# Performance work log

Hardware: AMD Instinct MI355X
Metric: run time of the kernel (lower is better)

## Reference

```python
import jax, jax.numpy as jnp
import numpy as np

B, J, I = 16, 96, 96
E, H = 256, 512
VS, VT = 32000, 32000
MAX_JUMP = 96
SJ = 2 * MAX_JUMP + 1  # 193
ALPHA_P0 = 0.3


def _lstm(x, W, b, reverse=False):
    """TF LSTMCell (gate order i, j, f, o; forget_bias=1.0). x: [B,J,E] -> [B,J,H]."""
    h_dim = W.shape[1] // 4
    xs = jnp.swapaxes(x, 0, 1)  # [J,B,E]
    if reverse:
        xs = xs[::-1]

    def step(carry, xt):
        h, c = carry
        z = jnp.concatenate([xt, h], axis=-1) @ W + b  # [B,4H]
        i, g, f, o = jnp.split(z, 4, axis=-1)
        c = jax.nn.sigmoid(f + 1.0) * c + jax.nn.sigmoid(i) * jnp.tanh(g)
        h = jax.nn.sigmoid(o) * jnp.tanh(c)
        return (h, c), h

    init = (jnp.zeros((x.shape[0], h_dim), x.dtype), jnp.zeros((x.shape[0], h_dim), x.dtype))
    _, hs = jax.lax.scan(step, init, xs)
    if reverse:
        hs = hs[::-1]
    return jnp.swapaxes(hs, 0, 1)


def setup_inputs() -> dict:
    key = jax.random.key(0)
    ks = jax.random.split(key, 16)
    s = 0.05
    return {
        "sources": jax.random.randint(ks[0], (B, I), 0, VS, dtype=jnp.int32),
        "targets": jax.random.randint(ks[1], (B, J), 0, VT, dtype=jnp.int32),
        "targets_null": jnp.array([VT - 1], dtype=jnp.int32),
        "emb": jax.random.normal(ks[2], (VT, E), jnp.float32) * s,
        "W_fw": jax.random.normal(ks[3], (E + H, 4 * H), jnp.float32) * s,
        "b_fw": jnp.zeros((4 * H,), jnp.float32),
        "W_bw": jax.random.normal(ks[4], (E + H, 4 * H), jnp.float32) * s,
        "b_bw": jnp.zeros((4 * H,), jnp.float32),
        "W_lstm": jax.random.normal(ks[5], (2 * H, E), jnp.float32) * s,
        "W1": jax.random.normal(ks[6], (E, H), jnp.float32) * s,
        "b1": jnp.zeros((H,), jnp.float32),
        "Wv": jax.random.normal(ks[7], (H, VS), jnp.float32) * s,
        "bv": jnp.zeros((VS,), jnp.float32),
        "Wj": jax.random.normal(ks[8], (H, SJ), jnp.float32) * s,
        "bj": jnp.zeros((SJ,), jnp.float32),
        "Wp": jax.random.normal(ks[9], (H, 1), jnp.float32) * s,
        "bp": jnp.zeros((1,), jnp.float32),
    }


def reference(sources, targets, targets_null, emb, W_fw, b_fw, W_bw, b_bw,
              W_lstm, W1, b1, Wv, bv, Wj, bj, Wp, bp):
    # shared target encoder (emission & transition use the same variables)
    e_word = emb[targets]          # [B,J,E]
    e_null = emb[targets_null]     # [1,E]
    h_fw = _lstm(e_word, W_fw, b_fw, reverse=False)
    h_bw = _lstm(e_word, W_bw, b_bw, reverse=True)
    ts = jnp.concatenate([h_fw, h_bw], axis=-1) @ W_lstm   # [B,J,E]
    ts = jnp.tanh(ts @ W1 + b1)                            # [B,J,H]
    tn = jnp.tanh(e_null @ W1 + b1)                        # [1,H]
    # keep_prob = 1.0 -> dropout is identity

    # ---- emission ----
    p_word = jax.nn.softmax(ts @ Wv + bv, axis=-1)         # [B,J,VS]
    p_null = jax.nn.softmax(tn @ Wv + bv, axis=-1)         # [1,VS]
    em_word = jnp.take_along_axis(p_word, sources[:, None, :], axis=2)  # [B,J,I]
    em_null = jnp.broadcast_to(p_null[0][sources][:, None, :], em_word.shape)  # tile over J
    emission_prob = jnp.concatenate([em_word, em_null], axis=1)  # [B,2J,I]

    # ---- transition ----
    jw = jax.nn.softmax(ts @ Wj + bj, axis=-1)             # [B,J,SJ]
    p0_scalar = jax.nn.sigmoid(tn @ Wp + bp)[0, 0] * ALPHA_P0
    p0 = jnp.broadcast_to(p0_scalar, (targets.shape[0], targets.shape[1]))  # [B,J]

    j_idx = jnp.arange(J)
    # window indices: for target word j, gather jw[j, MAX_JUMP - j + i] for i in [0,J)
    idx = MAX_JUMP - j_idx[:, None] + j_idx[None, :]       # [J,J]
    jww = jnp.take_along_axis(jw, idx[None, :, :], axis=2)  # [B,J,J]
    jww_sum = jnp.sum(jww, axis=-1, keepdims=True)
    jww_n = jww * (1.0 - p0[:, :, None]) / jww_sum          # normalized non-null jumps

    eye = jnp.eye(J, dtype=jww.dtype)
    half = jnp.concatenate([jww_n, p0[:, :, None] * eye], axis=2)       # [B,J,2J]
    transition = jnp.concatenate([half, half], axis=1)                  # [B,2J,2J]
    lhalf = jnp.concatenate([jnp.log(jww_n), jnp.log(p0)[:, :, None] * eye], axis=2)
    transition_log = jnp.concatenate([lhalf, lhalf], axis=1)            # [B,2J,2J]

    return emission_prob, transition, transition_log
```

## Files before the change

### kernel.cpp

```cpp
#include <hip/hip_runtime.h>
#include <math.h>

#define B_ 16
#define J_ 96
#define I_ 96
#define E_ 256
#define H_ 512
#define VS_ 32000
#define SJ_ 193
#define NROW (B_*J_)

typedef __attribute__((ext_vector_type(8))) short short8;
typedef __attribute__((ext_vector_type(4))) float f32x4;
typedef __attribute__((ext_vector_type(4))) unsigned int u32x4;

__device__ __forceinline__ float sigf(float x){ return 1.f/(1.f+__expf(-x)); }

__device__ __forceinline__ unsigned short f2bf(float x){
  unsigned int u = __float_as_uint(x);
  unsigned int r = (u + 0x7FFFu + ((u>>16)&1u)) >> 16;
  return (unsigned short)r;
}

#define ASYNC16(gp, lp) __builtin_amdgcn_global_load_lds( \
    (const __attribute__((address_space(1))) unsigned int*)(gp), \
    (__attribute__((address_space(3))) unsigned int*)(lp), 16, 0, 0)

__global__ void k_init(unsigned int* __restrict__ hex, float* __restrict__ rowsum){
  int i = blockIdx.x*256 + threadIdx.x;
  if (i < 32768) hex[i] = 0u;
  if (i < NROW + 1) rowsum[i] = 0.f;
}

__global__ void k_embed(const int* __restrict__ targets, const float* __restrict__ emb,
                        unsigned short* __restrict__ e_word_h){
  int row = blockIdx.x;
  int t = targets[row];
  e_word_h[(long long)row*E_ + threadIdx.x] = f2bf(emb[(long long)t*E_ + threadIdx.x]);
}

__device__ __forceinline__ void wtr_tile(const float* __restrict__ src,
                                         unsigned short* __restrict__ dst,
                                         int ldN, int nmax, int K, int n0, int k0,
                                         float* __restrict__ tile )
{
  const int t = threadIdx.x;
  #pragma unroll
  for (int rep = 0; rep < 8; rep++){
    int idx = rep*512 + t;
    int kk = idx >> 6, nn = idx & 63;
    tile[kk*65 + nn] = (n0+nn < nmax) ? src[(long long)(k0+kk)*ldN + n0 + nn] : 0.f;
  }
  __syncthreads();
  #pragma unroll
  for (int rep = 0; rep < 8; rep++){
    int idx = rep*512 + t;
    int nn = idx >> 6, kk = idx & 63;
    dst[(long long)(n0+nn)*K + k0 + kk] = f2bf(tile[kk*65 + nn]);
  }
}

__global__ __launch_bounds__(512, 2) void k_wtr2(const float* __restrict__ Wfw,
                                                 const float* __restrict__ Wbw,
                                                 unsigned short* __restrict__ WT){
  __shared__ float tile[64*65];
  int y = blockIdx.y;
  const float* src = y ? Wbw : Wfw;
  unsigned short* dst = WT + (long long)y*2048*256;
  int sid = blockIdx.x;
  int n0 = (sid & 31)*64, k0 = (sid >> 5)*64;
  wtr_tile(src, dst, 2048, 2048, 256, n0, k0, tile);
}

template<int MODE>
__global__ __launch_bounds__(256, 2) void k_bgemm(
    const unsigned short* __restrict__ Ah,
    const unsigned short* __restrict__ Bh,
    int K, int ncols,
    const float* __restrict__ bias,
    float* __restrict__ Cf,
    unsigned short* __restrict__ Ch,
    int ldc,
    float* __restrict__ rowsum)
{
  __shared__ unsigned short As[128*32];
  __shared__ unsigned short Bs[128*32];
  int nwg = gridDim.x;
  int braw = blockIdx.x;
  int wg = (braw & 7)*(nwg >> 3) + (braw >> 3);
  int mt = wg % 12, nt = wg / 12;
  const int m0 = mt*128, n0 = nt*128;
  const int t = threadIdx.x;
  const int lane = t & 63, w = t >> 6;
  const int wm = (w >> 1)*64, wn = (w & 1)*64;
  f32x4 acc[4][4] = {};
  for (int k0 = 0; k0 < K; k0 += 32){
    #pragma unroll
    for (int p = 0; p < 2; p++){
      int rowA = p*64 + (t >> 2);
      int kc = (t & 3) ^ ((rowA >> 1) & 3);
      const unsigned short* ga = Ah + (long long)(m0 + rowA)*K + k0 + kc*8;
      const unsigned short* gb = Bh + (long long)(n0 + rowA)*K + k0 + kc*8;
      unsigned short* la = As + p*2048 + w*512;
      unsigned short* lb = Bs + p*2048 + w*512;
      ASYNC16(ga, la);
      ASYNC16(gb, lb);
    }
    __syncthreads();
    short8 af[4], bf[4];
    const int rr = lane & 15, kch = lane >> 4;
    #pragma unroll
    for (int mi = 0; mi < 4; mi++){
      int rowA = wm + mi*16 + rr;
      int slot = kch ^ ((rowA >> 1) & 3);
      af[mi] = *(const short8*)&As[rowA*32 + slot*8];
    }
    #pragma unroll
    for (int ni = 0; ni < 4; ni++){
      int rowB = wn + ni*16 + rr;
      int slot = kch ^ ((rowB >> 1) & 3);
      bf[ni] = *(const short8*)&Bs[rowB*32 + slot*8];
    }
    #pragma unroll
    for (int mi = 0; mi < 4; mi++)
      #pragma unroll
      for (int ni = 0; ni < 4; ni++)
        acc[mi][ni] = __builtin_amdgcn_mfma_f32_16x16x32_bf16(af[mi], bf[ni], acc[mi][ni], 0, 0, 0);
    __syncthreads();
  }
  #pragma unroll
  for (int mi = 0; mi < 4; mi++){
    #pragma unroll
    for (int r = 0; r < 4; r++){
      int row = m0 + wm + mi*16 + ((lane >> 4) << 2) + r;
      if (MODE == 3){
        float s = 0.f;
        #pragma unroll
        for (int ni = 0; ni < 4; ni++){
          int col = n0 + wn + ni*16 + (lane & 15);
          s += __expf(acc[mi][ni][r] + bias[col]);
        }
        s += __shfl_xor(s, 1);
        s += __shfl_xor(s, 2);
        s += __shfl_xor(s, 4);
        s += __shfl_xor(s, 8);
        if ((lane & 15) == 0) atomicAdd(&rowsum[row], s);
      } else {
        #pragma unroll
        for (int ni = 0; ni < 4; ni++){
          int col = n0 + wn + ni*16 + (lane & 15);
          if (col >= ncols) continue;
          float v = acc[mi][ni][r] + (bias ? bias[col] : 0.f);
          if (MODE == 0){ Cf[(long long)row*ldc + col] = v; }
          if (MODE == 2){
            v = tanhf(v);
            if (Cf) Cf[(long long)row*ldc + col] = v;
            Ch[(long long)row*ldc + col] = f2bf(v);
          }
        }
      }
    }
  }
}

__global__ __launch_bounds__(512, 1) void k_fused(
    const float* __restrict__ Xfw, const float* __restrict__ Xbw,
    const float* __restrict__ Wfw, const float* __restrict__ Wbw,
    unsigned int* __restrict__ hex32,
    unsigned short* __restrict__ Hcat_h,
    const int* __restrict__ tnull, const float* __restrict__ emb,
    const float* __restrict__ W1, const float* __restrict__ b1,
    const float* __restrict__ Wp, const float* __restrict__ bp,
    const float* __restrict__ Wv, const float* __restrict__ bv,
    unsigned short* __restrict__ WvT,
    float* __restrict__ lognull, float* __restrict__ nullsum,
    float* __restrict__ p0,
    const float* __restrict__ Wl, unsigned short* __restrict__ W_comboT,
    const float* __restrict__ Wj, unsigned short* __restrict__ WjT)
{
  __shared__ __align__(16) unsigned short W_s[64*512];
  __shared__ __align__(16) float z_s[2][8][16][68];
  const int bid = blockIdx.x;
  const int t = threadIdx.x;

  if (bid >= 64){
    float* zflat = &z_s[0][0][0][0];
    int sid = bid - 64;
    if (sid == 0){
      float* en  = zflat;
      float* red = zflat + 256;
      if (t < E_) en[t] = emb[(long long)tnull[0]*E_ + t];
      __syncthreads();
      float s = b1[t];
      for (int e = 0; e < E_; e++) s += en[e]*W1[(long long)e*H_ + t];
      red[t] = tanhf(s)*Wp[t];
      __syncthreads();
      for (int w = 256; w > 0; w >>= 1){
        if (t < w) red[t] += red[t+w];
        __syncthreads();
      }
      if (t == 0) p0[0] = sigf(red[0] + bp[0])*0.3f;
      return;
    }
    sid -= 1;
    if (sid < 128){
      const int K8 = sid*8;
      float* WlS = zflat;
      #pragma unroll
      for (int rep = 0; rep < 4; rep++){
        int id = rep*512 + t;
        int kl = id >> 8, e = id & 255;
        WlS[kl*256 + e] = Wl[(long long)(K8 + kl)*256 + e];
      }
      __syncthreads();
      float acc[8] = {};
      for (int e = 0; e < 256; e++){
        float w1v = W1[(long long)e*512 + t];
        #pragma unroll
        for (int j = 0; j < 8; j++) acc[j] += WlS[j*256 + e]*w1v;
      }
      #pragma unroll
      for (int j = 0; j < 8; j++)
        W_comboT[(long long)t*1024 + K8 + j] = f2bf(acc[j]);
      return;
    }
    sid -= 128;
    if (sid < 32){
      wtr_tile(Wj, WjT, SJ_, SJ_, 512, (sid & 3)*64, (sid >> 2)*64, zflat);
      return;
    }
    sid -= 32;
    if (sid < 63){
      float* en  = zflat;
      float* tns = zflat + 256;
      float* red = zflat + 768;
      if (t < E_) en[t] = emb[(long long)tnull[0]*E_ + t];
      __syncthreads();
      float s0 = b1[t];
      for (int e = 0; e < E_; e++) s0 += en[e]*W1[(long long)e*H_ + t];
      tns[t] = tanhf(s0);
      __syncthreads();
      int c = sid*512 + t;
      float p = 0.f;
      if (c < VS_){
        float s = bv[c];
        for (int k = 0; k < H_; k++) s += tns[k]*Wv[(long long)k*VS_ + c];
        lognull[c] = s;
        p = __expf(s);
      }
      red[t] = p;
      __syncthreads();
      for (int w = 256; w > 0; w >>= 1){
        if (t < w) red[t] += red[t+w];
        __syncthreads();
      }
      if (t == 0) atomicAdd(nullsum, red[0]);
      return;
    }
    sid -= 63;
    wtr_tile(Wv, WvT, VS_, VS_, H_, (sid % 500)*64, (sid / 500)*64, zflat);
    return;
  }

  const int dir = bid >> 5;
  const int slice = bid & 31;
  const int u0 = slice * 16;
  const int lane = t & 63;
  const int w = t >> 6;
  const int m = lane & 15, hi = lane >> 4;
  const float* X = dir ? Xbw : Xfw;
  const float* Wg = (dir ? Wbw : Wfw) + (long long)E_*2048;
  char* hexd = (char*)hex32 + dir*65536;

  for (int rep = 0; rep < 8; rep++){
    int id = rep*512 + t;
    int k = id >> 3, col8 = (id & 7)*8;
    int g = col8 >> 4, uu0 = col8 & 15;
    const float* src = Wg + (long long)k*2048 + g*512 + u0 + uu0;
    float4 w0 = *(const float4*)src;
    float4 w1 = *(const float4*)(src + 4);
    float wv8[8] = {w0.x,w0.y,w0.z,w0.w,w1.x,w1.y,w1.z,w1.w};
    #pragma unroll
    for (int j = 0; j < 8; j++){
      int c = col8 + j;
      int byte = (c << 10) + (k << 1);
      byte ^= ((c & 7) << 4);
      *(unsigned short*)((char*)W_s + byte) = f2bf(wv8[j]);
    }
  }
  __syncthreads();

  short8 bfr[4][2];
  #pragma unroll
  for (int nt = 0; nt < 4; nt++)
    #pragma unroll
    for (int ck = 0; ck < 2; ck++){
      int col = nt*16 + m;
      int kc = 2*w + ck;
      int byte = (col << 10) + kc*64 + hi*16;
      byte ^= ((col & 7) << 4);
      bfr[nt][ck] = *(const short8*)((const char*)W_s + byte);
    }

  const int eb = t >> 4, eu = t & 15;
  float creg = 0.f;

  for (int step = 0; step < J_; step++){
    const int par = step & 1;
    const int t_eff = dir ? (J_-1-step) : step;
    float xg0=0.f, xg1=0.f, xg2=0.f, xg3=0.f;
    if (t < 256){
      const float* xr = X + ((long long)eb*J_ + t_eff)*2048 + u0 + eu;
      xg0 = xr[0]; xg1 = xr[512]; xg2 = xr[1024]; xg3 = xr[1536];
      asm volatile("" : "+v"(xg0), "+v"(xg1), "+v"(xg2), "+v"(xg3));
    }
    const char* ap = hexd + par*32768 + m*2048 + w*256 + hi*32;
    u32x4 d0, d1, d2, d3;
    const unsigned expt = (unsigned)step;
    unsigned spin = 0;
    for (;;){
      asm volatile("global_load_dwordx4 %0, %1, off sc0 sc1" : "=v"(d0) : "v"(ap));
      asm volatile("global_load_dwordx4 %0, %1, off offset:16 sc0 sc1" : "=v"(d1) : "v"(ap));
      asm volatile("global_load_dwordx4 %0, %1, off offset:128 sc0 sc1" : "=v"(d2) : "v"(ap));
      asm volatile("global_load_dwordx4 %0, %1, off offset:144 sc0 sc1" : "=v"(d3) : "v"(ap));
      asm volatile("s_waitcnt vmcnt(0)" ::: "memory");
      unsigned bad = (d0[1]^expt)|(d0[3]^expt)|(d1[1]^expt)|(d1[3]^expt)
                   | (d2[1]^expt)|(d2[3]^expt)|(d3[1]^expt)|(d3[3]^expt);
      if (__all(bad == 0u)) break;
      if (++spin > 65536u) break;
      __builtin_amdgcn_s_sleep(1);
    }
    __builtin_amdgcn_sched_barrier(0);
    union { unsigned int u[4]; short8 s; } a0, a1;
    a0.u[0]=d0[0]; a0.u[1]=d0[2]; a0.u[2]=d1[0]; a0.u[3]=d1[2];
    a1.u[0]=d2[0]; a1.u[1]=d2[2]; a1.u[2]=d3[0]; a1.u[3]=d3[2];
    f32x4 acc[4] = {{0.f,0.f,0.f,0.f},{0.f,0.f,0.f,0.f},{0.f,0.f,0.f,0.f},{0.f,0.f,0.f,0.f}};
    #pragma unroll
    for (int nt = 0; nt < 4; nt++){
      acc[nt] = __builtin_amdgcn_mfma_f32_16x16x32_bf16(a0.s, bfr[nt][0], acc[nt], 0,0,0);
      acc[nt] = __builtin_amdgcn_mfma_f32_16x16x32_bf16(a1.s, bfr[nt][1], acc[nt], 0,0,0);
    }
    #pragma unroll
    for (int nt = 0; nt < 4; nt++)
      #pragma unroll
      for (int r = 0; r < 4; r++)
        z_s[par][w][hi*4 + r][nt*16 + m] = acc[nt][r];
    __syncthreads();
    if (t < 256){
      float z0 = xg0, z1 = xg1, z2 = xg2, z3 = xg3;
      #pragma unroll
      for (int ke = 0; ke < 8; ke++){
        z0 += z_s[par][ke][eb][eu];
        z1 += z_s[par][ke][eb][16 + eu];
        z2 += z_s[par][ke][eb][32 + eu];
        z3 += z_s[par][ke][eb][48 + eu];
      }
      creg = sigf(z2 + 1.f)*creg + sigf(z0)*tanhf(z1);
      float hh = sigf(z3)*tanhf(creg);
      unsigned int hb16 = (unsigned int)f2bf(hh);
      unsigned int nb = (unsigned int)__shfl_xor((int)hb16, 1);
      if (!(eu & 1)){
        unsigned long long pkt = (unsigned long long)((hb16 & 0xffffu) | (nb << 16))
                               | ((unsigned long long)(unsigned)(step+1) << 32);
        __hip_atomic_store((unsigned long long*)(hexd + (par^1)*32768 + eb*2048 + (u0 + eu)*4),
                           pkt, __ATOMIC_RELAXED, __HIP_MEMORY_SCOPE_AGENT);
      }
      Hcat_h[((long long)eb*J_ + t_eff)*1024 + dir*512 + u0 + eu] = (unsigned short)hb16;
    }
  }
}

__global__ __launch_bounds__(64, 8) void k_glgemm(
    const unsigned short* __restrict__ t1h,
    const unsigned short* __restrict__ WvT,
    const float* __restrict__ bv,
    const int* __restrict__ sources,
    const float* __restrict__ rowsum,
    float* __restrict__ out_em)
{
  const int bx = blockIdx.x;
  const int b = bx / 36, tile = bx % 36;
  const int mt = tile / 6, nt = tile % 6;
  const int lane = threadIdx.x;
  const int rr = lane & 15, kq = lane >> 4;
  int s = sources[b*96 + nt*16 + rr];
  float bg = bv[s];
  const unsigned short* arow = t1h + ((long long)(b*96 + mt*16 + rr))*512 + kq*8;
  const unsigned short* brow = WvT + (long long)s*512 + kq*8;
  f32x4 acc = {0.f,0.f,0.f,0.f};
  #pragma unroll
  for (int kc = 0; kc < 16; kc++){
    short8 af = *(const short8*)(arow + kc*32);
    short8 bf = *(const short8*)(brow + kc*32);
    acc = __builtin_amdgcn_mfma_f32_16x16x32_bf16(af, bf, acc, 0, 0, 0);
  }
  #pragma unroll
  for (int r = 0; r < 4; r++){
    int j = mt*16 + kq*4 + r;
    int i = nt*16 + rr;
    float v = __expf(acc[r] + bg) / rowsum[b*96 + j];
    out_em[((long long)b*192 + j)*96 + i] = v;
  }
}

__global__ void k_emission_null(const float* __restrict__ lognull,
                                const float* __restrict__ nullsum,
                                const int* __restrict__ sources,
                                float* __restrict__ out_em){
  int b = blockIdx.x;
  int i = threadIdx.x;
  if (i >= 96) return;
  int s = sources[b*96 + i];
  float v = __expf(lognull[s]) / nullsum[0];
  for (int jj = 0; jj < 96; jj++)
    out_em[((long long)b*192 + 96 + jj)*96 + i] = v;
}

__global__ void k_transition(const float* __restrict__ jlog, const float* __restrict__ p0p,
                             float* __restrict__ T, float* __restrict__ TL){
  int bx = blockIdx.x;
  int b = bx / J_, j = bx % J_;
  int tid = threadIdx.x;
  __shared__ float ex[128];
  __shared__ float red[128];
  float e = 0.f;
  if (tid < 96) e = __expf(jlog[(long long)bx*SJ_ + (96 - j + tid)]);
  ex[tid] = e; red[tid] = e;
  __syncthreads();
  for (int w = 64; w > 0; w >>= 1){
    if (tid < w) red[tid] += red[tid+w];
    __syncthreads();
  }
  float p0 = p0p[0];
  float scale = (1.f - p0) / red[0];
  float lp0 = logf(p0);
  long long r0 = ((long long)b*192 + j)*192;
  long long r1 = ((long long)b*192 + j + 96)*192;
  for (int col = tid; col < 192; col += 128){
    float tv, lv;
    if (col < 96){ tv = ex[col]*scale; lv = logf(tv); }
    else { bool d = (col - 96) == j; tv = d ? p0 : 0.f; lv = d ? lp0 : 0.f; }
    T[r0 + col] = tv; T[r1 + col] = tv;
    TL[r0 + col] = lv; TL[r1 + col] = lv;
  }
}

extern "C" void kernel_launch(void* const* d_in, const int* in_sizes, int n_in,
                              void* d_out, int out_size, void* d_ws, size_t ws_size,
                              hipStream_t stream)
{
  const int* sources = (const int*)d_in[0];
  const int* targets = (const int*)d_in[1];
  const int* tnull   = (const int*)d_in[2];
  const float* emb   = (const float*)d_in[3];
  const float* Wfw   = (const float*)d_in[4];
  const float* bfw   = (const float*)d_in[5];
  const float* Wbw   = (const float*)d_in[6];
  const float* bbw   = (const float*)d_in[7];
  const float* Wl    = (const float*)d_in[8];
  const float* W1    = (const float*)d_in[9];
  const float* b1    = (const float*)d_in[10];
  const float* Wv    = (const float*)d_in[11];
  const float* bv    = (const float*)d_in[12];
  const float* Wj    = (const float*)d_in[13];
  const float* bj    = (const float*)d_in[14];
  const float* Wp    = (const float*)d_in[15];
  const float* bp    = (const float*)d_in[16];
  float* out = (float*)d_out;
  float* ws  = (float*)d_ws;

  long long off = 0;
  float* Xfw    = ws + off; off += (long long)NROW*2048;
  float* Xbw    = ws + off; off += (long long)NROW*2048;
  unsigned short* e_word_h = (unsigned short*)(ws + off); off += (long long)NROW*E_/2;
  unsigned short* WT       = (unsigned short*)(ws + off); off += 2LL*2048*256/2;
  unsigned short* Hcat_h   = (unsigned short*)(ws + off); off += (long long)NROW*1024/2;
  unsigned int* hex32 = (unsigned int*)(ws + off); off += 32768;
  unsigned short* t1h = (unsigned short*)(ws + off); off += (long long)NROW*H_/2;
  unsigned short* W_comboT = (unsigned short*)(ws + off); off += 512LL*1024/2;
  unsigned short* WjT      = (unsigned short*)(ws + off); off += 256LL*512/2;
  float* rowsum = ws + off; off += NROW;
  float* nullsum= ws + off; off += 1;
  float* p0     = ws + off; off += 1;
  float* lognull= ws + off; off += VS_;
  float* jlog   = ws + off; off += (long long)NROW*SJ_;
  unsigned short* WvT = (unsigned short*)(ws + off); off += (long long)VS_*H_/2;

  float* out_em = out;
  float* out_T  = out + (long long)B_*192*96;
  float* out_TL = out_T + (long long)B_*192*192;

  k_init<<<128, 256, 0, stream>>>(hex32, rowsum);

  k_embed<<<NROW, 256, 0, stream>>>(targets, emb, e_word_h);
  k_wtr2<<<dim3(128, 2), 512, 0, stream>>>(Wfw, Wbw, WT);

  k_bgemm<0><<<192, 256, 0, stream>>>(e_word_h, WT,            E_, 2048, bfw, Xfw, nullptr, 2048, nullptr);
  k_bgemm<0><<<192, 256, 0, stream>>>(e_word_h, WT + 2048*256, E_, 2048, bbw, Xbw, nullptr, 2048, nullptr);

  k_fused<<<4288, 512, 0, stream>>>(Xfw, Xbw, Wfw, Wbw, hex32, Hcat_h,
                                    tnull, emb, W1, b1, Wp, bp, Wv, bv,
                                    WvT, lognull, nullsum, p0,
                                    Wl, W_comboT, Wj, WjT);

  k_bgemm<2><<<48, 256, 0, stream>>>(Hcat_h, W_comboT, 2*H_, H_, b1, nullptr, t1h, H_, nullptr);

  k_bgemm<0><<<24, 256, 0, stream>>>(t1h, WjT, H_, SJ_, bj, jlog, nullptr, SJ_, nullptr);

  k_bgemm<3><<<3000, 256, 0, stream>>>(t1h, WvT, H_, VS_, bv, nullptr, nullptr, VS_, rowsum);

  k_glgemm<<<576, 64, 0, stream>>>(t1h, WvT, bv, sources, rowsum, out_em);

  k_emission_null<<<B_, 128, 0, stream>>>(lognull, nullsum, sources, out_em);
  k_transition<<<NROW, 128, 0, stream>>>(jlog, p0, out_T, out_TL);
}
```

Before: 483.5 us.

## Merge small launches into fused head, mega GEMM, and final kernels; double-buffer spin poll

Collapses init, embed, and weight-transpose into one head kernel, and batches the two input-projection GEMMs into a single 2D launch. The jump GEMM, vocab row-sum GEMM, and gathered emission GEMM now share one mega launch, and the null-emission and transition kernels merge into one final kernel that also applies the softmax normalization. The LSTM spin-wait loop now keeps two sets of loads in flight so polling overlaps with the flag check. The aim is to cut launch count and tail idle time. The cost is that division by rowsum moves to a separate read-modify-write pass over the emission output.

Result: slower. 565.3 us (+16.9%).

```diff
diff --git a/kernel.cpp b/kernel.cpp
--- a/kernel.cpp
+++ b/kernel.cpp
@@ -26,23 +26,31 @@
     (const __attribute__((address_space(1))) unsigned int*)(gp), \
     (__attribute__((address_space(3))) unsigned int*)(lp), 16, 0, 0)
 
-__global__ void k_init(unsigned int* __restrict__ hex, float* __restrict__ rowsum){
-  int i = blockIdx.x*256 + threadIdx.x;
-  if (i < 32768) hex[i] = 0u;
-  if (i < NROW + 1) rowsum[i] = 0.f;
-}
-
-__global__ void k_embed(const int* __restrict__ targets, const float* __restrict__ emb,
-                        unsigned short* __restrict__ e_word_h){
-  int row = blockIdx.x;
-  int t = targets[row];
-  e_word_h[(long long)row*E_ + threadIdx.x] = f2bf(emb[(long long)t*E_ + threadIdx.x]);
+__device__ __forceinline__ void wtr_tile256(const float* __restrict__ src,
+                                            unsigned short* __restrict__ dst,
+                                            int ldN, int nmax, int K, int n0, int k0,
+                                            float* __restrict__ tile )
+{
+  const int t = threadIdx.x;
+  #pragma unroll
+  for (int rep = 0; rep < 16; rep++){
+    int idx = rep*256 + t;
+    int kk = idx >> 6, nn = idx & 63;
+    tile[kk*65 + nn] = (n0+nn < nmax) ? src[(long long)(k0+kk)*ldN + n0 + nn] : 0.f;
+  }
+  __syncthreads();
+  #pragma unroll
+  for (int rep = 0; rep < 16; rep++){
+    int idx = rep*256 + t;
+    int nn = idx >> 6, kk = idx & 63;
+    dst[(long long)(n0+nn)*K + k0 + kk] = f2bf(tile[kk*65 + nn]);
+  }
 }
 
 __device__ __forceinline__ void wtr_tile(const float* __restrict__ src,
                                          unsigned short* __restrict__ dst,
                                          int ldN, int nmax, int K, int n0, int k0,
-                                         float* __restrict__ tile )
+                                         float* __restrict__ tile)
 {
   const int t = threadIdx.x;
   #pragma unroll
@@ -60,16 +68,88 @@
   }
 }
 
-__global__ __launch_bounds__(512, 2) void k_wtr2(const float* __restrict__ Wfw,
-                                                 const float* __restrict__ Wbw,
-                                                 unsigned short* __restrict__ WT){
+__global__ __launch_bounds__(256) void k_head(
+    const int* __restrict__ targets, const float* __restrict__ emb,
+    unsigned short* __restrict__ e_word_h,
+    const float* __restrict__ Wfw, const float* __restrict__ Wbw,
+    unsigned short* __restrict__ WT,
+    unsigned int* __restrict__ hex, float* __restrict__ rowsum,
+    const float* __restrict__ bfw, const float* __restrict__ bbw,
+    float* __restrict__ wsb)
+{
   __shared__ float tile[64*65];
-  int y = blockIdx.y;
-  const float* src = y ? Wbw : Wfw;
-  unsigned short* dst = WT + (long long)y*2048*256;
-  int sid = blockIdx.x;
-  int n0 = (sid & 31)*64, k0 = (sid >> 5)*64;
-  wtr_tile(src, dst, 2048, 2048, 256, n0, k0, tile);
+  int bid = blockIdx.x;
+  const int t = threadIdx.x;
+  if (bid < 1536){
+    int tr = targets[bid];
+    e_word_h[(long long)bid*E_ + t] = f2bf(emb[(long long)tr*E_ + t]);
+    return;
+  }
+  bid -= 1536;
+  if (bid < 256){
+    int y = bid >> 7;
+    const float* src = y ? Wbw : Wfw;
+    unsigned short* dst = WT + (long long)y*2048*256;
+    int sid = bid & 127;
+    wtr_tile256(src, dst, 2048, 2048, 256, (sid & 31)*64, (sid >> 5)*64, tile);
+    return;
+  }
+  bid -= 256;
+  if (bid < 128){ hex[bid*256 + t] = 0u; return; }
+  bid -= 128;
+  if (bid < 7){
+    int i = bid*256 + t;
+    if (i < NROW + 1) rowsum[i] = 0.f;
+    return;
+  }
+  bid -= 7;
+  int i = bid*256 + t;
+  wsb[i] = (i < 2048) ? bfw[i] : bbw[i - 2048];
+}
+
+__device__ __forceinline__ void gemm128(const unsigned short* __restrict__ Ah,
+                                        const unsigned short* __restrict__ Bh,
+                                        int K, int m0, int n0,
+                                        unsigned short* As, unsigned short* Bs,
+                                        f32x4 (&acc)[4][4])
+{
+  const int t = threadIdx.x;
+  const int lane = t & 63, w = t >> 6;
+  const int wm = (w >> 1)*64, wn = (w & 1)*64;
+  for (int k0 = 0; k0 < K; k0 += 32){
+    #pragma unroll
+    for (int p = 0; p < 2; p++){
+      int rowA = p*64 + (t >> 2);
+      int kc = (t & 3) ^ ((rowA >> 1) & 3);
+      const unsigned short* ga = Ah + (long long)(m0 + rowA)*K + k0 + kc*8;
+      const unsigned short* gb = Bh + (long long)(n0 + rowA)*K + k0 + kc*8;
+      unsigned short* la = As + p*2048 + w*512;
+      unsigned short* lb = Bs + p*2048 + w*512;
+      ASYNC16(ga, la);
+      ASYNC16(gb, lb);
+    }
+    __syncthreads();
+    short8 af[4], bf[4];
+    const int rr = lane & 15, kch = lane >> 4;
+    #pragma unroll
+    for (int mi = 0; mi < 4; mi++){
+      int rowA = wm + mi*16 + rr;
+      int slot = kch ^ ((rowA >> 1) & 3);
+      af[mi] = *(const short8*)&As[rowA*32 + slot*8];
+    }
+    #pragma unroll
+    for (int ni = 0; ni < 4; ni++){
+      int rowB = wn + ni*16 + rr;
+      int slot = kch ^ ((rowB >> 1) & 3);
+      bf[ni] = *(const short8*)&Bs[rowB*32 + slot*8];
+    }
+    #pragma unroll
+    for (int mi = 0; mi < 4; mi++)
+      #pragma unroll
+      for (int ni = 0; ni < 4; ni++)
+        acc[mi][ni] = __builtin_amdgcn_mfma_f32_16x16x32_bf16(af[mi], bf[ni], acc[mi][ni], 0, 0, 0);
+    __syncthreads();
+  }
 }
 
 template<int MODE>
@@ -81,82 +161,41 @@
     float* __restrict__ Cf,
     unsigned short* __restrict__ Ch,
     int ldc,
-    float* __restrict__ rowsum)
+    long long sB2, long long sBias2, long long sC2)
 {
   __shared__ unsigned short As[128*32];
   __shared__ unsigned short Bs[128*32];
+  if (blockIdx.y){
+    Bh += sB2;
+    if (bias) bias += sBias2;
+    if (Cf) Cf += sC2;
+    if (Ch) Ch += sC2;
+  }
   int nwg = gridDim.x;
   int braw = blockIdx.x;
   int wg = (braw & 7)*(nwg >> 3) + (braw >> 3);
   int mt = wg % 12, nt = wg / 12;
   const int m0 = mt*128, n0 = nt*128;
+  f32x4 acc[4][4] = {};
+  gemm128(Ah, Bh, K, m0, n0, As, Bs, acc);
   const int t = threadIdx.x;
   const int lane = t & 63, w = t >> 6;
   const int wm = (w >> 1)*64, wn = (w & 1)*64;
-  f32x4 acc[4][4] = {};
-  for (int k0 = 0; k0 < K; k0 += 32){
-    #pragma unroll
-    for (int p = 0; p < 2; p++){
-      int rowA = p*64 + (t >> 2);
-      int kc = (t & 3) ^ ((rowA >> 1) & 3);
-      const unsigned short* ga = Ah + (long long)(m0 + rowA)*K + k0 + kc*8;
-      const unsigned short* gb = Bh + (long long)(n0 + rowA)*K + k0 + kc*8;
-      unsigned short* la = As + p*2048 + w*512;
-      unsigned short* lb = Bs + p*2048 + w*512;
-      ASYNC16(ga, la);
-      ASYNC16(gb, lb);
-    }
-    __syncthreads();
-    short8 af[4], bf[4];
-    const int rr = lane & 15, kch = lane >> 4;
-    #pragma unroll
-    for (int mi = 0; mi < 4; mi++){
-      int rowA = wm + mi*16 + rr;
-      int slot = kch ^ ((rowA >> 1) & 3);
-      af[mi] = *(const short8*)&As[rowA*32 + slot*8];
-    }
-    #pragma unroll
-    for (int ni = 0; ni < 4; ni++){
-      int rowB = wn + ni*16 + rr;
-      int slot = kch ^ ((rowB >> 1) & 3);
-      bf[ni] = *(const short8*)&Bs[rowB*32 + slot*8];
-    }
-    #pragma unroll
-    for (int mi = 0; mi < 4; mi++)
-      #pragma unroll
-      for (int ni = 0; ni < 4; ni++)
-        acc[mi][ni] = __builtin_amdgcn_mfma_f32_16x16x32_bf16(af[mi], bf[ni], acc[mi][ni], 0, 0, 0);
-    __syncthreads();
-  }
   #pragma unroll
   for (int mi = 0; mi < 4; mi++){
     #pragma unroll
     for (int r = 0; r < 4; r++){
       int row = m0 + wm + mi*16 + ((lane >> 4) << 2) + r;
-      if (MODE == 3){
-        float s = 0.f;
-        #pragma unroll
-        for (int ni = 0; ni < 4; ni++){
-          int col = n0 + wn + ni*16 + (lane & 15);
-          s += __expf(acc[mi][ni][r] + bias[col]);
-        }
-        s += __shfl_xor(s, 1);
-        s += __shfl_xor(s, 2);
-        s += __shfl_xor(s, 4);
-        s += __shfl_xor(s, 8);
-        if ((lane & 15) == 0) atomicAdd(&rowsum[row], s);
-      } else {
-        #pragma unroll
-        for (int ni = 0; ni < 4; ni++){
-          int col = n0 + wn + ni*16 + (lane & 15);
-          if (col >= ncols) continue;
-          float v = acc[mi][ni][r] + (bias ? bias[col] : 0.f);
-          if (MODE == 0){ Cf[(long long)row*ldc + col] = v; }
-          if (MODE == 2){
-            v = tanhf(v);
-            if (Cf) Cf[(long long)row*ldc + col] = v;
-            Ch[(long long)row*ldc + col] = f2bf(v);
-          }
+      #pragma unroll
+      for (int ni = 0; ni < 4; ni++){
+        int col = n0 + wn + ni*16 + (lane & 15);
+        if (col >= ncols) continue;
+        float v = acc[mi][ni][r] + (bias ? bias[col] : 0.f);
+        if (MODE == 0){ Cf[(long long)row*ldc + col] = v; }
+        if (MODE == 2){
+          v = tanhf(v);
+          if (Cf) Cf[(long long)row*ldc + col] = v;
+          Ch[(long long)row*ldc + col] = f2bf(v);
         }
       }
     }
@@ -315,25 +354,45 @@
       asm volatile("" : "+v"(xg0), "+v"(xg1), "+v"(xg2), "+v"(xg3));
     }
     const char* ap = hexd + par*32768 + m*2048 + w*256 + hi*32;
-    u32x4 d0, d1, d2, d3;
+    u32x4 dA0, dA1, dA2, dA3, dB0, dB1, dB2, dB3;
     const unsigned expt = (unsigned)step;
     unsigned spin = 0;
+    bool gotA = true;
+    asm volatile("global_load_dwordx4 %0, %1, off sc0 sc1" : "=v"(dA0) : "v"(ap));
+    asm volatile("global_load_dwordx4 %0, %1, off offset:16 sc0 sc1" : "=v"(dA1) : "v"(ap));
+    asm volatile("global_load_dwordx4 %0, %1, off offset:128 sc0 sc1" : "=v"(dA2) : "v"(ap));
+    asm volatile("global_load_dwordx4 %0, %1, off offset:144 sc0 sc1" : "=v"(dA3) : "v"(ap));
     for (;;){
-      asm volatile("global_load_dwordx4 %0, %1, off sc0 sc1" : "=v"(d0) : "v"(ap));
-      asm volatile("global_load_dwordx4 %0, %1, off offset:16 sc0 sc1" : "=v"(d1) : "v"(ap));
-      asm volatile("global_load_dwordx4 %0, %1, off offset:128 sc0 sc1" : "=v"(d2) : "v"(ap));
-      asm volatile("global_load_dwordx4 %0, %1, off offset:144 sc0 sc1" : "=v"(d3) : "v"(ap));
-      asm volatile("s_waitcnt vmcnt(0)" ::: "memory");
-      unsigned bad = (d0[1]^expt)|(d0[3]^expt)|(d1[1]^expt)|(d1[3]^expt)
-                   | (d2[1]^expt)|(d2[3]^expt)|(d3[1]^expt)|(d3[3]^expt);
-      if (__all(bad == 0u)) break;
-      if (++spin > 65536u) break;
-      __builtin_amdgcn_s_sleep(1);
-    }
+      asm volatile("global_load_dwordx4 %0, %1, off sc0 sc1" : "=v"(dB0) : "v"(ap));
+      asm volatile("global_load_dwordx4 %0, %1, off offset:16 sc0 sc1" : "=v"(dB1) : "v"(ap));
+      asm volatile("global_load_dwordx4 %0, %1, off offset:128 sc0 sc1" : "=v"(dB2) : "v"(ap));
+      asm volatile("global_load_dwordx4 %0, %1, off offset:144 sc0 sc1" : "=v"(dB3) : "v"(ap));
+      asm volatile("s_waitcnt vmcnt(4)" ::: "memory");
+      __builtin_amdgcn_sched_barrier(0);
+      unsigned bad = (dA0[1]^expt)|(dA0[3]^expt)|(dA1[1]^expt)|(dA1[3]^expt)
+                   | (dA2[1]^expt)|(dA2[3]^expt)|(dA3[1]^expt)|(dA3[3]^expt);
+      if (__all(bad == 0u)){ gotA = true; break; }
+      asm volatile("global_load_dwordx4 %0, %1, off sc0 sc1" : "=v"(dA0) : "v"(ap));
+      asm volatile("global_load_dwordx4 %0, %1, off offset:16 sc0 sc1" : "=v"(dA1) : "v"(ap));
+      asm volatile("global_load_dwordx4 %0, %1, off offset:128 sc0 sc1" : "=v"(dA2) : "v"(ap));
+      asm volatile("global_load_dwordx4 %0, %1, off offset:144 sc0 sc1" : "=v"(dA3) : "v"(ap));
+      asm volatile("s_waitcnt vmcnt(4)" ::: "memory");
+      __builtin_amdgcn_sched_barrier(0);
+      bad = (dB0[1]^expt)|(dB0[3]^expt)|(dB1[1]^expt)|(dB1[3]^expt)
+          | (dB2[1]^expt)|(dB2[3]^expt)|(dB3[1]^expt)|(dB3[3]^expt);
+      if (__all(bad == 0u)){ gotA = false; break; }
+      if ((spin += 2) > 65536u){ gotA = true; break; }
+    }
+    asm volatile("s_waitcnt vmcnt(0)" ::: "memory");
     __builtin_amdgcn_sched_barrier(0);
     union { unsigned int u[4]; short8 s; } a0, a1;
-    a0.u[0]=d0[0]; a0.u[1]=d0[2]; a0.u[2]=d1[0]; a0.u[3]=d1[2];
-    a1.u[0]=d2[0]; a1.u[1]=d2[2]; a1.u[2]=d3[0]; a1.u[3]=d3[2];
+    if (gotA){
+      a0.u[0]=dA0[0]; a0.u[1]=dA0[2]; a0.u[2]=dA1[0]; a0.u[3]=dA1[2];
+      a1.u[0]=dA2[0]; a1.u[1]=dA2[2]; a1.u[2]=dA3[0]; a1.u[3]=dA3[2];
+    } else {
+      a0.u[0]=dB0[0]; a0.u[1]=dB0[2]; a0.u[2]=dB1[0]; a0.u[3]=dB1[2];
+      a1.u[0]=dB2[0]; a1.u[1]=dB2[2]; a1.u[2]=dB3[0]; a1.u[3]=dB3[2];
+    }
     f32x4 acc[4] = {{0.f,0.f,0.f,0.f},{0.f,0.f,0.f,0.f},{0.f,0.f,0.f,0.f},{0.f,0.f,0.f,0.f}};
     #pragma unroll
     for (int nt = 0; nt < 4; nt++){
@@ -370,59 +429,112 @@
   }
 }
 
-__global__ __launch_bounds__(64, 8) void k_glgemm(
+__global__ __launch_bounds__(256, 2) void k_mega(
     const unsigned short* __restrict__ t1h,
     const unsigned short* __restrict__ WvT,
-    const float* __restrict__ bv,
+    const unsigned short* __restrict__ WjT,
+    const float* __restrict__ bv, const float* __restrict__ bj,
     const int* __restrict__ sources,
+    float* __restrict__ rowsum, float* __restrict__ jlog,
+    float* __restrict__ out_em)
+{
+  __shared__ unsigned short As[128*32];
+  __shared__ unsigned short Bs[128*32];
+  const int t = threadIdx.x;
+  const int lane = t & 63, w = t >> 6;
+  int bid = blockIdx.x;
+  if (bid >= 3024){
+    int tile = (bid - 3024)*4 + w;
+    int b = tile / 36, tl = tile % 36;
+    int mt = tl / 6, nt = tl % 6;
+    const int rr = lane & 15, kq = lane >> 4;
+    int s = sources[b*96 + nt*16 + rr];
+    float bg = bv[s];
+    const unsigned short* arow = t1h + ((long long)(b*96 + mt*16 + rr))*512 + kq*8;
+    const unsigned short* brow = WvT + (long long)s*512 + kq*8;
+    f32x4 acc = {0.f,0.f,0.f,0.f};
+    #pragma unroll
+    for (int kc = 0; kc < 16; kc++){
+      short8 af = *(const short8*)(arow + kc*32);
+      short8 bf = *(const short8*)(brow + kc*32);
+      acc = __builtin_amdgcn_mfma_f32_16x16x32_bf16(af, bf, acc, 0, 0, 0);
+    }
+    #pragma unroll
+    for (int r = 0; r < 4; r++){
+      int j = mt*16 + kq*4 + r;
+      int i = nt*16 + rr;
+      out_em[((long long)b*192 + j)*96 + i] = __expf(acc[r] + bg);
+    }
+    return;
+  }
+  const bool isjl = (bid >= 3000);
+  int m0, n0;
+  const unsigned short* Bh;
+  if (isjl){
+    int idx = bid - 3000;
+    m0 = (idx % 12)*128; n0 = (idx / 12)*128;
+    Bh = WjT;
+  } else {
+    int wg = (bid & 7)*375 + (bid >> 3);
+    m0 = (wg % 12)*128; n0 = (wg / 12)*128;
+    Bh = WvT;
+  }
+  f32x4 acc[4][4] = {};
+  gemm128(t1h, Bh, H_, m0, n0, As, Bs, acc);
+  const int wm = (w >> 1)*64, wn = (w & 1)*64;
+  #pragma unroll
+  for (int mi = 0; mi < 4; mi++){
+    #pragma unroll
+    for (int r = 0; r < 4; r++){
+      int row = m0 + wm + mi*16 + ((lane >> 4) << 2) + r;
+      if (isjl){
+        #pragma unroll
+        for (int ni = 0; ni < 4; ni++){
+          int col = n0 + wn + ni*16 + (lane & 15);
+          if (col < SJ_) jlog[(long long)row*SJ_ + col] = acc[mi][ni][r] + bj[col];
+        }
+      } else {
+        float s = 0.f;
+        #pragma unroll
+        for (int ni = 0; ni < 4; ni++){
+          int col = n0 + wn + ni*16 + (lane & 15);
+          s += __expf(acc[mi][ni][r] + bv[col]);
+        }
+        s += __shfl_xor(s, 1);
+        s += __shfl_xor(s, 2);
+        s += __shfl_xor(s, 4);
+        s += __shfl_xor(s, 8);
+        if ((lane & 15) == 0) atomicAdd(&rowsum[row], s);
+      }
+    }
+  }
+}
+
+__global__ __launch_bounds__(128) void k_final(
+    const float* __restrict__ jlog, const float* __restrict__ p0p,
     const float* __restrict__ rowsum,
-    float* __restrict__ out_em)
-{
-  const int bx = blockIdx.x;
-  const int b = bx / 36, tile = bx % 36;
-  const int mt = tile / 6, nt = tile % 6;
-  const int lane = threadIdx.x;
-  const int rr = lane & 15, kq = lane >> 4;
-  int s = sources[b*96 + nt*16 + rr];
-  float bg = bv[s];
-  const unsigned short* arow = t1h + ((long long)(b*96 + mt*16 + rr))*512 + kq*8;
-  const unsigned short* brow = WvT + (long long)s*512 + kq*8;
-  f32x4 acc = {0.f,0.f,0.f,0.f};
-  #pragma unroll
-  for (int kc = 0; kc < 16; kc++){
-    short8 af = *(const short8*)(arow + kc*32);
-    short8 bf = *(const short8*)(brow + kc*32);
-    acc = __builtin_amdgcn_mfma_f32_16x16x32_bf16(af, bf, acc, 0, 0, 0);
-  }
-  #pragma unroll
-  for (int r = 0; r < 4; r++){
-    int j = mt*16 + kq*4 + r;
-    int i = nt*16 + rr;
-    float v = __expf(acc[r] + bg) / rowsum[b*96 + j];
-    out_em[((long long)b*192 + j)*96 + i] = v;
-  }
-}
-
-__global__ void k_emission_null(const float* __restrict__ lognull,
-                                const float* __restrict__ nullsum,
-                                const int* __restrict__ sources,
-                                float* __restrict__ out_em){
-  int b = blockIdx.x;
-  int i = threadIdx.x;
-  if (i >= 96) return;
-  int s = sources[b*96 + i];
-  float v = __expf(lognull[s]) / nullsum[0];
-  for (int jj = 0; jj < 96; jj++)
-    out_em[((long long)b*192 + 96 + jj)*96 + i] = v;
-}
-
-__global__ void k_transition(const float* __restrict__ jlog, const float* __restrict__ p0p,
-                             float* __restrict__ T, float* __restrict__ TL){
-  int bx = blockIdx.x;
-  int b = bx / J_, j = bx % J_;
-  int tid = threadIdx.x;
+    const float* __restrict__ lognull, const float* __restrict__ nullsum,
+    const int* __restrict__ sources,
+    float* __restrict__ out_em, float* __restrict__ T, float* __restrict__ TL)
+{
   __shared__ float ex[128];
   __shared__ float red[128];
+  int bx = blockIdx.x;
+  int tid = threadIdx.x;
+  if (bx >= NROW){
+    int b = bx - NROW;
+    if (tid < 96){
+      int s = sources[b*96 + tid];
+      float v = __expf(lognull[s]) / nullsum[0];
+      for (int jj = 0; jj < 96; jj++)
+        out_em[((long long)b*192 + 96 + jj)*96 + tid] = v;
+    }
+    return;
+  }
+  int b = bx / J_, j = bx % J_;
+  float inv = 1.f / rowsum[bx];
+  if (tid < 96)
+    out_em[((long long)b*192 + j)*96 + tid] *= inv;
   float e = 0.f;
   if (tid < 96) e = __expf(jlog[(long long)bx*SJ_ + (96 - j + tid)]);
   ex[tid] = e; red[tid] = e;
@@ -482,6 +594,7 @@
   float* rowsum = ws + off; off += NROW;
   float* nullsum= ws + off; off += 1;
   float* p0     = ws + off; off += 1;
+  float* wsb    = ws + off; off += 4096;
   float* lognull= ws + off; off += VS_;
   float* jlog   = ws + off; off += (long long)NROW*SJ_;
   unsigned short* WvT = (unsigned short*)(ws + off); off += (long long)VS_*H_/2;
@@ -490,27 +603,24 @@
   float* out_T  = out + (long long)B_*192*96;
   float* out_TL = out_T + (long long)B_*192*192;
 
-  k_init<<<128, 256, 0, stream>>>(hex32, rowsum);
-
-  k_embed<<<NROW, 256, 0, stream>>>(targets, emb, e_word_h);
-  k_wtr2<<<dim3(128, 2), 512, 0, stream>>>(Wfw, Wbw, WT);
-
-  k_bgemm<0><<<192, 256, 0, stream>>>(e_word_h, WT,            E_, 2048, bfw, Xfw, nullptr, 2048, nullptr);
-  k_bgemm<0><<<192, 256, 0, stream>>>(e_word_h, WT + 2048*256, E_, 2048, bbw, Xbw, nullptr, 2048, nullptr);
+  k_head<<<1943, 256, 0, stream>>>(targets, emb, e_word_h, Wfw, Wbw, WT,
+                                   hex32, rowsum, bfw, bbw, wsb);
+
+  k_bgemm<0><<<dim3(192, 2), 256, 0, stream>>>(e_word_h, WT, E_, 2048, wsb,
+                                               Xfw, nullptr, 2048,
+                                               2048LL*256, 2048LL, (long long)NROW*2048);
 
   k_fused<<<4288, 512, 0, stream>>>(Xfw, Xbw, Wfw, Wbw, hex32, Hcat_h,
                                     tnull, emb, W1, b1, Wp, bp, Wv, bv,
                                     WvT, lognull, nullsum, p0,
                                     Wl, W_comboT, Wj, WjT);
 
-  k_bgemm<2><<<48, 256, 0, stream>>>(Hcat_h, W_comboT, 2*H_, H_, b1, nullptr, t1h, H_, nullptr);
-
-  k_bgemm<0><<<24, 256, 0, stream>>>(t1h, WjT, H_, SJ_, bj, jlog, nullptr, SJ_, nullptr);
-
-  k_bgemm<3><<<3000, 256, 0, stream>>>(t1h, WvT, H_, VS_, bv, nullptr, nullptr, VS_, rowsum);
-
-  k_glgemm<<<576, 64, 0, stream>>>(t1h, WvT, bv, sources, rowsum, out_em);
-
-  k_emission_null<<<B_, 128, 0, stream>>>(lognull, nullsum, sources, out_em);
-  k_transition<<<NROW, 128, 0, stream>>>(jlog, p0, out_T, out_TL);
-}
+  k_bgemm<2><<<dim3(48, 1), 256, 0, stream>>>(Hcat_h, W_comboT, 2*H_, H_, b1,
+                                              nullptr, t1h, H_, 0, 0, 0);
+
+  k_mega<<<3168, 256, 0, stream>>>(t1h, WvT, WjT, bv, bj, sources,
+                                   rowsum, jlog, out_em);
+
+  k_final<<<NROW + B_, 128, 0, stream>>>(jlog, p0, rowsum, lognull, nullsum,
+                                         sources, out_em, out_T, out_TL);
+}
```
